# Kernel optimization log

Measured on AMD Instinct MI355X. Metric: run time of the kernel, lower is better.

Reference implementation:

```python
import jax, jax.numpy as jnp
import numpy as np

NUM_HARMONICS = 64
TEMPERATURE = 1.0

def setup_inputs() -> dict:
    key = jax.random.key(0)
    k1, k2 = jax.random.split(key)
    phases_q = jax.random.normal(k1, (2, 8, 2048, NUM_HARMONICS), dtype=jnp.float32)
    phases_k = jax.random.normal(k2, (2, 8, 2048, NUM_HARMONICS), dtype=jnp.float32)
    return {"phases_q": phases_q, "phases_k": phases_k}

def reference(phases_q, phases_k):
    # mean_h cos(q_h - k_h) = (cos_q @ cos_k^T + sin_q @ sin_k^T) / H
    # (identity: cos(a-b) = cos a cos b + sin a sin b) -- avoids the
    # O(Sq*Sk*H) broadcast intermediate of the naive formulation.
    cq, sq = jnp.cos(phases_q), jnp.sin(phases_q)
    ck, sk = jnp.cos(phases_k), jnp.sin(phases_k)
    coherence = (jnp.einsum('bhqd,bhkd->bhqk', cq, ck) +
                 jnp.einsum('bhqd,bhkd->bhqk', sq, sk)) / NUM_HARMONICS
    return coherence / TEMPERATURE
```

## Files before the change

kernel.cpp:

```cpp
#include <hip/hip_runtime.h>
#include <hip/hip_bf16.h>

#define SEQ 2048
#define NH  64
#define KP  128
#define NBATCH 16

typedef __attribute__((ext_vector_type(8))) short  short8;
typedef __attribute__((ext_vector_type(4))) float  floatx4;

static __device__ __forceinline__ unsigned short f2bf(float f) {
    union { float f; unsigned u; } x; x.f = f;
    return (unsigned short)((x.u + 0x7fffu + ((x.u >> 16) & 1u)) >> 16);
}

__global__ void sincos_pack_kernel(const float* __restrict__ pq,
                                   const float* __restrict__ pk,
                                   unsigned short* __restrict__ qpack,
                                   unsigned short* __restrict__ kpack) {
    int i = blockIdx.x * blockDim.x + threadIdx.x;
    const float* src = blockIdx.y ? pk : pq;
    unsigned short* dst = blockIdx.y ? kpack : qpack;
    float4 v = ((const float4*)src)[i];
    int base = i << 2;
    int row  = base >> 6;
    int h    = base & 63;
    float s0, c0, s1, c1, s2, c2, s3, c3;
    __sincosf(v.x, &s0, &c0);
    __sincosf(v.y, &s1, &c1);
    __sincosf(v.z, &s2, &c2);
    __sincosf(v.w, &s3, &c3);
    ushort4 cu; cu.x = f2bf(c0); cu.y = f2bf(c1); cu.z = f2bf(c2); cu.w = f2bf(c3);
    ushort4 su; su.x = f2bf(s0); su.y = f2bf(s1); su.z = f2bf(s2); su.w = f2bf(s3);
    unsigned short* p = dst + (size_t)row * KP + h;
    *(ushort4*)p        = cu;
    *(ushort4*)(p + NH) = su;
}

__global__ __launch_bounds__(256, 2)
void coherence_gemm_kernel(const unsigned short* __restrict__ Qp,
                           const unsigned short* __restrict__ Kp,
                           float* __restrict__ out) {
    __shared__ unsigned short As[128 * KP];
    __shared__ unsigned short Bs[128 * KP];
    const int b  = blockIdx.z;
    const int tm = blockIdx.y;
    const int tn = blockIdx.x;
    const int tid  = threadIdx.x;
    const int wave = tid >> 6;
    const int lane = tid & 63;

    const size_t qbase = (size_t)b * SEQ * KP + (size_t)tm * 128 * KP;
    const size_t kbase = (size_t)b * SEQ * KP + (size_t)tn * 128 * KP;
    const int subrow = lane >> 4;
    const int cslot  = lane & 15;
    for (int it = 0; it < 8; ++it) {
        const int rg = wave * 32 + it * 4;
        const int r  = rg + subrow;
        const int cg = cslot ^ (r & 7);
        const unsigned short* gA = Qp + qbase + (size_t)r * KP + cg * 8;
        const unsigned short* gB = Kp + kbase + (size_t)r * KP + cg * 8;
        unsigned short* lA = As + rg * KP;
        unsigned short* lB = Bs + rg * KP;
        __builtin_amdgcn_global_load_lds(
            (const __attribute__((address_space(1))) void*)gA,
            (__attribute__((address_space(3))) void*)lA, 16, 0, 0);
        __builtin_amdgcn_global_load_lds(
            (const __attribute__((address_space(1))) void*)gB,
            (__attribute__((address_space(3))) void*)lB, 16, 0, 0);
    }
    __syncthreads();

    const int wr = wave >> 1, wc = wave & 1;
    const int qlane = lane >> 4;
    const int mrow  = lane & 15;

    floatx4 acc[4][4] = {};
    #pragma unroll
    for (int ks = 0; ks < 4; ++ks) {
        short8 af[4], bf[4];
        #pragma unroll
        for (int im = 0; im < 4; ++im) {
            const int m = wr * 64 + im * 16 + mrow;
            const int chunk = (ks * 4 + qlane) ^ (m & 7);
            af[im] = *(const short8*)(As + m * KP + chunk * 8);
        }
        #pragma unroll
        for (int in = 0; in < 4; ++in) {
            const int n = wc * 64 + in * 16 + mrow;
            const int chunk = (ks * 4 + qlane) ^ (n & 7);
            bf[in] = *(const short8*)(Bs + n * KP + chunk * 8);
        }
        #pragma unroll
        for (int im = 0; im < 4; ++im)
            #pragma unroll
            for (int in = 0; in < 4; ++in)
                acc[im][in] = __builtin_amdgcn_mfma_f32_16x16x32_bf16(
                    af[im], bf[in], acc[im][in], 0, 0, 0);
    }

    const size_t obase = (size_t)b * SEQ * SEQ + (size_t)(tm * 128) * SEQ + tn * 128;
    const float scale = 1.0f / 64.0f;
    #pragma unroll
    for (int im = 0; im < 4; ++im) {
        #pragma unroll
        for (int in = 0; in < 4; ++in) {
            const int n = wc * 64 + in * 16 + mrow;
            #pragma unroll
            for (int j = 0; j < 4; ++j) {
                const int m = wr * 64 + im * 16 + qlane * 4 + j;
                out[obase + (size_t)m * SEQ + n] = acc[im][in][j] * scale;
            }
        }
    }
}

extern "C" void kernel_launch(void* const* d_in, const int* in_sizes, int n_in,
                              void* d_out, int out_size, void* d_ws, size_t ws_size,
                              hipStream_t stream) {
    const float* pq = (const float*)d_in[0];
    const float* pk = (const float*)d_in[1];
    float* out = (float*)d_out;

    unsigned short* qpack = (unsigned short*)d_ws;
    unsigned short* kpack = qpack + (size_t)NBATCH * SEQ * KP;

    const int n4 = NBATCH * SEQ * NH / 4;
    dim3 pgrid(n4 / 256, 2, 1);
    sincos_pack_kernel<<<pgrid, 256, 0, stream>>>(pq, pk, qpack, kpack);

    dim3 ggrid(SEQ / 128, SEQ / 128, NBATCH);
    coherence_gemm_kernel<<<ggrid, 256, 0, stream>>>(qpack, kpack, out);
}
```

Before: 294.6 us.

## Use 512-thread blocks, swap MFMA operands for vectorized nontemporal output stores

Doubles the GEMM block to 8 waves. Four waves now load the Q tile and four load the K tile, and each wave computes a 64x32 sub-tile. The MFMA operands are swapped so each lane holds four consecutive output columns, which lets the epilogue write a float4 with a nontemporal store instead of scalar strided stores. The goal is to cut the cost of writing the large fp32 output and to raise occupancy, at the price of more waves competing for LDS bandwidth.

```diff
diff --git a/kernel.cpp b/kernel.cpp
--- a/kernel.cpp
+++ b/kernel.cpp
@@ -37,7 +37,7 @@
     *(ushort4*)(p + NH) = su;
 }
 
-__global__ __launch_bounds__(256, 2)
+__global__ __launch_bounds__(512, 4)
 void coherence_gemm_kernel(const unsigned short* __restrict__ Qp,
                            const unsigned short* __restrict__ Kp,
                            float* __restrict__ out) {
@@ -54,31 +54,31 @@
     const size_t kbase = (size_t)b * SEQ * KP + (size_t)tn * 128 * KP;
     const int subrow = lane >> 4;
     const int cslot  = lane & 15;
+    const bool isB = wave >= 4;
+    const unsigned short* gsrc = isB ? (Kp + kbase) : (Qp + qbase);
+    unsigned short* ldst = isB ? Bs : As;
+    const int w4 = wave & 3;
+    #pragma unroll
     for (int it = 0; it < 8; ++it) {
-        const int rg = wave * 32 + it * 4;
+        const int rg = w4 * 32 + it * 4;
         const int r  = rg + subrow;
         const int cg = cslot ^ (r & 7);
-        const unsigned short* gA = Qp + qbase + (size_t)r * KP + cg * 8;
-        const unsigned short* gB = Kp + kbase + (size_t)r * KP + cg * 8;
-        unsigned short* lA = As + rg * KP;
-        unsigned short* lB = Bs + rg * KP;
+        const unsigned short* g = gsrc + (size_t)r * KP + cg * 8;
+        unsigned short* l = ldst + rg * KP;
         __builtin_amdgcn_global_load_lds(
-            (const __attribute__((address_space(1))) void*)gA,
-            (__attribute__((address_space(3))) void*)lA, 16, 0, 0);
-        __builtin_amdgcn_global_load_lds(
-            (const __attribute__((address_space(1))) void*)gB,
-            (__attribute__((address_space(3))) void*)lB, 16, 0, 0);
+            (const __attribute__((address_space(1))) void*)g,
+            (__attribute__((address_space(3))) void*)l, 16, 0, 0);
     }
     __syncthreads();
 
-    const int wr = wave >> 1, wc = wave & 1;
+    const int wr = wave >> 2, wc = wave & 3;
     const int qlane = lane >> 4;
     const int mrow  = lane & 15;
 
-    floatx4 acc[4][4] = {};
+    floatx4 acc[4][2] = {};
     #pragma unroll
     for (int ks = 0; ks < 4; ++ks) {
-        short8 af[4], bf[4];
+        short8 af[4], bf[2];
         #pragma unroll
         for (int im = 0; im < 4; ++im) {
             const int m = wr * 64 + im * 16 + mrow;
@@ -86,31 +86,30 @@
             af[im] = *(const short8*)(As + m * KP + chunk * 8);
         }
         #pragma unroll
-        for (int in = 0; in < 4; ++in) {
-            const int n = wc * 64 + in * 16 + mrow;
+        for (int in = 0; in < 2; ++in) {
+            const int n = wc * 32 + in * 16 + mrow;
             const int chunk = (ks * 4 + qlane) ^ (n & 7);
             bf[in] = *(const short8*)(Bs + n * KP + chunk * 8);
         }
         #pragma unroll
         for (int im = 0; im < 4; ++im)
             #pragma unroll
-            for (int in = 0; in < 4; ++in)
+            for (int in = 0; in < 2; ++in)
                 acc[im][in] = __builtin_amdgcn_mfma_f32_16x16x32_bf16(
-                    af[im], bf[in], acc[im][in], 0, 0, 0);
+                    bf[in], af[im], acc[im][in], 0, 0, 0);
     }
 
     const size_t obase = (size_t)b * SEQ * SEQ + (size_t)(tm * 128) * SEQ + tn * 128;
     const float scale = 1.0f / 64.0f;
     #pragma unroll
     for (int im = 0; im < 4; ++im) {
+        const int m = wr * 64 + im * 16 + mrow;
         #pragma unroll
-        for (int in = 0; in < 4; ++in) {
-            const int n = wc * 64 + in * 16 + mrow;
-            #pragma unroll
-            for (int j = 0; j < 4; ++j) {
-                const int m = wr * 64 + im * 16 + qlane * 4 + j;
-                out[obase + (size_t)m * SEQ + n] = acc[im][in][j] * scale;
-            }
+        for (int in = 0; in < 2; ++in) {
+            const int n0 = wc * 32 + in * 16 + qlane * 4;
+            floatx4 v = acc[im][in] * scale;
+            __builtin_nontemporal_store(
+                v, (floatx4*)(out + obase + (size_t)m * SEQ + n0));
         }
     }
 }
@@ -130,5 +129,5 @@
     sincos_pack_kernel<<<pgrid, 256, 0, stream>>>(pq, pk, qpack, kpack);
 
     dim3 ggrid(SEQ / 128, SEQ / 128, NBATCH);
-    coherence_gemm_kernel<<<ggrid, 256, 0, stream>>>(qpack, kpack, out);
+    coherence_gemm_kernel<<<ggrid, 512, 0, stream>>>(qpack, kpack, out);
 }
```

Result: slower. 302.3 us (+2.6%).
